# Optimization experiments

Hardware: AMD Instinct MI355X
Metric: run time of the kernel (lower is better)

## Reference

```python
import jax, jax.numpy as jnp
import numpy as np

N, T, F, D, E = 50000, 16, 128, 128, 1_600_000


def setup_inputs() -> dict:
    key = jax.random.key(0)
    k0, k1, k2, k3 = jax.random.split(key, 4)
    x = jax.random.normal(k0, (N, T, F), dtype=jnp.float32)
    edge_index = jax.random.randint(k1, (2, E), 0, N, dtype=jnp.int64)
    W_conv = jax.random.normal(k2, (F, D), dtype=jnp.float32) * 0.05
    b_conv = jnp.zeros((D,), dtype=jnp.float32)
    W_lin = jax.random.normal(k3, (D, D), dtype=jnp.float32) * 0.05
    b_lin = jnp.zeros((D,), dtype=jnp.float32)
    return {"x": x, "edge_index": edge_index, "W_conv": W_conv,
            "b_conv": b_conv, "W_lin": W_lin, "b_lin": b_lin}


def reference(x, edge_index, W_conv, b_conv, W_lin, b_lin):
    n = x.shape[0]
    loop = jnp.arange(n, dtype=edge_index.dtype)
    # GCNConv with add_self_loops=True (PyG semantics)
    src = jnp.concatenate([edge_index[0], loop])  # [E+N]
    dst = jnp.concatenate([edge_index[1], loop])  # [E+N]
    deg = jax.ops.segment_sum(jnp.ones_like(src, dtype=x.dtype), dst,
                              num_segments=n)
    dinv = jnp.where(deg > 0, jax.lax.rsqrt(deg), 0.0)
    norm = (dinv[src] * dinv[dst])[:, None]  # symmetric normalization

    def step(h_prev, xt):
        xw = xt @ W_conv                        # [N, D]
        agg = jax.ops.segment_sum(xw[src] * norm, dst, num_segments=n)
        h = jnp.tanh(agg + b_conv + h_prev @ W_lin + b_lin)
        return h, h

    h0 = jnp.zeros((n, W_conv.shape[1]), dtype=x.dtype)
    _, hs = jax.lax.scan(step, h0, jnp.swapaxes(x, 0, 1))  # hs: [T, N, D]
    return jnp.swapaxes(hs, 0, 1)  # [N, T, D]
```

## Files before the change

kernel.cpp:

```cpp
#include <hip/hip_runtime.h>
#include <math.h>

#define NN 50000
#define TT 16
#define DD 128
#define MT (NN * TT)
#define SCAN_B 1024
#define SCAN_NB ((NN + SCAN_B - 1) / SCAN_B)

typedef __attribute__((ext_vector_type(8))) short short8;
typedef __attribute__((ext_vector_type(4))) float f32x4;

static __device__ __forceinline__ unsigned short f2bf(float f) {
  unsigned u = __float_as_uint(f);
  u += 0x7FFFu + ((u >> 16) & 1u);
  return (unsigned short)(u >> 16);
}
static __device__ __forceinline__ float bf_lo(unsigned v) {
  return __uint_as_float(v << 16);
}
static __device__ __forceinline__ float bf_hi(unsigned v) {
  return __uint_as_float(v & 0xffff0000u);
}


__global__ void k_init(int* __restrict__ deg, int* __restrict__ cur) {
  int i = blockIdx.x * blockDim.x + threadIdx.x;
  if (i < NN) { deg[i] = 1; cur[i] = 0; }
}

__global__ void k_deg_count(const int* __restrict__ dst, int* __restrict__ deg, int e) {
  int i = blockIdx.x * blockDim.x + threadIdx.x;
  if (i < e) atomicAdd(&deg[dst[i]], 1);
}

__global__ __launch_bounds__(SCAN_B) void k_scan1(const int* __restrict__ deg,
                                                  int* __restrict__ rowptr,
                                                  int* __restrict__ bsums,
                                                  float* __restrict__ dinv) {
  __shared__ int sm[SCAN_B];
  int tid = threadIdx.x;
  int i = blockIdx.x * SCAN_B + tid;
  int d = (i < NN) ? deg[i] : 1;
  if (i < NN) dinv[i] = rsqrtf((float)d);
  int v = d - 1;
  sm[tid] = v;
  __syncthreads();
  for (int off = 1; off < SCAN_B; off <<= 1) {
    int t = (tid >= off) ? sm[tid - off] : 0;
    __syncthreads();
    sm[tid] += t;
    __syncthreads();
  }
  if (i < NN) rowptr[i] = sm[tid] - v;
  if (tid == SCAN_B - 1) bsums[blockIdx.x] = sm[tid];
}

__global__ void k_scan2(int* __restrict__ bsums) {
  __shared__ int sm[64];
  int tid = threadIdx.x;
  int v = (tid < SCAN_NB) ? bsums[tid] : 0;
  sm[tid] = v;
  __syncthreads();
  for (int off = 1; off < 64; off <<= 1) {
    int t = (tid >= off) ? sm[tid - off] : 0;
    __syncthreads();
    sm[tid] += t;
    __syncthreads();
  }
  if (tid < SCAN_NB) bsums[tid] = sm[tid] - v;
  if (tid == 63) bsums[SCAN_NB] = sm[63];
}

__global__ __launch_bounds__(SCAN_B) void k_scan3(int* __restrict__ rowptr,
                                                  const int* __restrict__ bsums) {
  int i = blockIdx.x * SCAN_B + threadIdx.x;
  if (i < NN) rowptr[i] += bsums[blockIdx.x];
  if (i == 0) rowptr[NN] = bsums[SCAN_NB];
}

__global__ void k_fill(const int* __restrict__ src, const int* __restrict__ dst,
                       const int* __restrict__ rowptr, int* __restrict__ cur,
                       int* __restrict__ col, int e) {
  int i = blockIdx.x * blockDim.x + threadIdx.x;
  if (i < e) {
    int d = dst[i];
    int slot = atomicAdd(&cur[d], 1);
    col[rowptr[d] + slot] = src[i];
  }
}

__global__ void k_wprep(const float* __restrict__ Wc, const float* __restrict__ Wl,
                        const float* __restrict__ bc, const float* __restrict__ bl,
                        unsigned short* __restrict__ Wct, unsigned short* __restrict__ Wlt,
                        float* __restrict__ bsum) {
  int n = blockIdx.x, k = threadIdx.x;
  Wct[n * 128 + k] = f2bf(Wc[k * 128 + n]);
  Wlt[n * 128 + k] = f2bf(Wl[k * 128 + n]);
  if (n == 0) bsum[k] = bc[k] + bl[k];
}

__global__ __launch_bounds__(256) void k_gemmx(
    const float* __restrict__ X, const unsigned short* __restrict__ Wct,
    const float* __restrict__ dinv, char* __restrict__ Yq, float* __restrict__ scaleN)
{
  __shared__ unsigned short sA[128 * 136];
  const int tid = threadIdx.x;
  const long row0 = (long)blockIdx.x * 128;

  {
    const float4* xp = (const float4*)(X + row0 * 128);
    #pragma unroll
    for (int it = 0; it < 16; ++it) {
      float4 v = xp[it * 256 + tid];
      int q = it * 256 + tid;
      int r = q >> 5;
      int k = (q & 31) * 4;
      unsigned u0 = (unsigned)f2bf(v.x) | ((unsigned)f2bf(v.y) << 16);
      unsigned u1 = (unsigned)f2bf(v.z) | ((unsigned)f2bf(v.w) << 16);
      *(uint2*)&sA[r * 136 + k] = make_uint2(u0, u1);
    }
  }
  __syncthreads();

  const int w = tid >> 6, l = tid & 63;
  const int lr = l & 15;
  const int lk = (l >> 4) << 3;
  f32x4 acc[2][8];
  #pragma unroll
  for (int i = 0; i < 2; ++i)
    #pragma unroll
    for (int n = 0; n < 8; ++n) acc[i][n] = (f32x4){0.f, 0.f, 0.f, 0.f};

  #pragma unroll
  for (int kg = 0; kg < 4; ++kg) {
    int kb = kg * 32 + lk;
    short8 a0 = *(const short8*)&sA[(w * 32 + lr) * 136 + kb];
    short8 a1 = *(const short8*)&sA[(w * 32 + 16 + lr) * 136 + kb];
    #pragma unroll
    for (int n = 0; n < 8; ++n) {
      short8 b = *(const short8*)&Wct[(n * 16 + lr) * 128 + kb];
      acc[0][n] = __builtin_amdgcn_mfma_f32_16x16x32_bf16(b, a0, acc[0][n], 0, 0, 0);
      acc[1][n] = __builtin_amdgcn_mfma_f32_16x16x32_bf16(b, a1, acc[1][n], 0, 0, 0);
    }
  }

  const int wb = (l >> 4) * 4;
  #pragma unroll
  for (int i = 0; i < 2; ++i) {
    const long rbase = row0 + w * 32 + i * 16;
    const int node = (int)(rbase >> 4);
    const long row = rbase + lr;
    float m = 0.f;
    #pragma unroll
    for (int n = 0; n < 8; ++n)
      #pragma unroll
      for (int r = 0; r < 4; ++r) m = fmaxf(m, fabsf(acc[i][n][r]));
    #pragma unroll
    for (int mask = 1; mask < 64; mask <<= 1)
      m = fmaxf(m, __shfl_xor(m, mask, 64));
    const float f = (m > 0.f) ? 127.f / m : 0.f;
    if (l == 0) scaleN[node] = m * dinv[node] * (1.f / 127.f);
    #pragma unroll
    for (int n = 0; n < 8; ++n) {
      int q0 = (int)__builtin_rintf(acc[i][n][0] * f);
      int q1 = (int)__builtin_rintf(acc[i][n][1] * f);
      int q2 = (int)__builtin_rintf(acc[i][n][2] * f);
      int q3 = (int)__builtin_rintf(acc[i][n][3] * f);
      unsigned u = (unsigned)(q0 & 255) | ((unsigned)(q1 & 255) << 8) |
                   ((unsigned)(q2 & 255) << 16) | ((unsigned)(q3 & 255) << 24);
      *(unsigned*)(Yq + row * 128 + n * 16 + wb) = u;
    }
  }
}

__global__ __launch_bounds__(256) void k_gatherN(
    const uint2* __restrict__ Yq,
    const float* __restrict__ scaleN,
    const int* __restrict__ col, const int* __restrict__ rowptr,
    const float* __restrict__ dinv, const float* __restrict__ bsum,
    unsigned* __restrict__ aggT)
{
  const int n = blockIdx.x;
  const int tid = threadIdx.x;
  float a0 = 0, a1 = 0, a2 = 0, a3 = 0, a4 = 0, a5 = 0, a6 = 0, a7 = 0;
  {
    uint2 v = Yq[(long)n * 256 + tid];
    float ss = scaleN[n];
    a0 = fmaf((float)(signed char)(v.x),       ss, a0);
    a1 = fmaf((float)(signed char)(v.x >> 8),  ss, a1);
    a2 = fmaf((float)(signed char)(v.x >> 16), ss, a2);
    a3 = fmaf((float)(signed char)(v.x >> 24), ss, a3);
    a4 = fmaf((float)(signed char)(v.y),       ss, a4);
    a5 = fmaf((float)(signed char)(v.y >> 8),  ss, a5);
    a6 = fmaf((float)(signed char)(v.y >> 16), ss, a6);
    a7 = fmaf((float)(signed char)(v.y >> 24), ss, a7);
  }
  int j = rowptr[n];
  const int end = rowptr[n + 1];
  for (; j + 4 <= end; j += 4) {
    int s0 = col[j], s1 = col[j + 1], s2 = col[j + 2], s3 = col[j + 3];
    float c0 = scaleN[s0], c1 = scaleN[s1], c2 = scaleN[s2], c3 = scaleN[s3];
    uint2 v0 = Yq[(long)s0 * 256 + tid];
    uint2 v1 = Yq[(long)s1 * 256 + tid];
    uint2 v2 = Yq[(long)s2 * 256 + tid];
    uint2 v3 = Yq[(long)s3 * 256 + tid];
    a0 = fmaf((float)(signed char)(v0.x),       c0, a0);
    a1 = fmaf((float)(signed char)(v0.x >> 8),  c0, a1);
    a2 = fmaf((float)(signed char)(v0.x >> 16), c0, a2);
    a3 = fmaf((float)(signed char)(v0.x >> 24), c0, a3);
    a4 = fmaf((float)(signed char)(v0.y),       c0, a4);
    a5 = fmaf((float)(signed char)(v0.y >> 8),  c0, a5);
    a6 = fmaf((float)(signed char)(v0.y >> 16), c0, a6);
    a7 = fmaf((float)(signed char)(v0.y >> 24), c0, a7);
    a0 = fmaf((float)(signed char)(v1.x),       c1, a0);
    a1 = fmaf((float)(signed char)(v1.x >> 8),  c1, a1);
    a2 = fmaf((float)(signed char)(v1.x >> 16), c1, a2);
    a3 = fmaf((float)(signed char)(v1.x >> 24), c1, a3);
    a4 = fmaf((float)(signed char)(v1.y),       c1, a4);
    a5 = fmaf((float)(signed char)(v1.y >> 8),  c1, a5);
    a6 = fmaf((float)(signed char)(v1.y >> 16), c1, a6);
    a7 = fmaf((float)(signed char)(v1.y >> 24), c1, a7);
    a0 = fmaf((float)(signed char)(v2.x),       c2, a0);
    a1 = fmaf((float)(signed char)(v2.x >> 8),  c2, a1);
    a2 = fmaf((float)(signed char)(v2.x >> 16), c2, a2);
    a3 = fmaf((float)(signed char)(v2.x >> 24), c2, a3);
    a4 = fmaf((float)(signed char)(v2.y),       c2, a4);
    a5 = fmaf((float)(signed char)(v2.y >> 8),  c2, a5);
    a6 = fmaf((float)(signed char)(v2.y >> 16), c2, a6);
    a7 = fmaf((float)(signed char)(v2.y >> 24), c2, a7);
    a0 = fmaf((float)(signed char)(v3.x),       c3, a0);
    a1 = fmaf((float)(signed char)(v3.x >> 8),  c3, a1);
    a2 = fmaf((float)(signed char)(v3.x >> 16), c3, a2);
    a3 = fmaf((float)(signed char)(v3.x >> 24), c3, a3);
    a4 = fmaf((float)(signed char)(v3.y),       c3, a4);
    a5 = fmaf((float)(signed char)(v3.y >> 8),  c3, a5);
    a6 = fmaf((float)(signed char)(v3.y >> 16), c3, a6);
    a7 = fmaf((float)(signed char)(v3.y >> 24), c3, a7);
  }
  for (; j < end; ++j) {
    int s = col[j];
    float cs = scaleN[s];
    uint2 v = Yq[(long)s * 256 + tid];
    a0 = fmaf((float)(signed char)(v.x),       cs, a0);
    a1 = fmaf((float)(signed char)(v.x >> 8),  cs, a1);
    a2 = fmaf((float)(signed char)(v.x >> 16), cs, a2);
    a3 = fmaf((float)(signed char)(v.x >> 24), cs, a3);
    a4 = fmaf((float)(signed char)(v.y),       cs, a4);
    a5 = fmaf((float)(signed char)(v.y >> 8),  cs, a5);
    a6 = fmaf((float)(signed char)(v.y >> 16), cs, a6);
    a7 = fmaf((float)(signed char)(v.y >> 24), cs, a7);
  }
  const int t = tid >> 4, dq = tid & 15;
  const float di = dinv[n];
  const float4 b0 = *(const float4*)&bsum[dq * 8];
  const float4 b1 = *(const float4*)&bsum[dq * 8 + 4];
  a0 = fmaf(a0, di, b0.x); a1 = fmaf(a1, di, b0.y);
  a2 = fmaf(a2, di, b0.z); a3 = fmaf(a3, di, b0.w);
  a4 = fmaf(a4, di, b1.x); a5 = fmaf(a5, di, b1.y);
  a6 = fmaf(a6, di, b1.z); a7 = fmaf(a7, di, b1.w);
  unsigned u0 = (unsigned)f2bf(a0) | ((unsigned)f2bf(a1) << 16);
  unsigned u1 = (unsigned)f2bf(a2) | ((unsigned)f2bf(a3) << 16);
  unsigned u2 = (unsigned)f2bf(a4) | ((unsigned)f2bf(a5) << 16);
  unsigned u3 = (unsigned)f2bf(a6) | ((unsigned)f2bf(a7) << 16);
  unsigned* ap = aggT + ((long)t * NN + n) * 64 + dq * 4;
  __builtin_nontemporal_store(u0, ap);
  __builtin_nontemporal_store(u1, ap + 1);
  __builtin_nontemporal_store(u2, ap + 2);
  __builtin_nontemporal_store(u3, ap + 3);
}

__global__ __launch_bounds__(64) void k_rnn(
    const unsigned* __restrict__ aggT,
    const unsigned short* __restrict__ Wlt,
    float* __restrict__ out)
{
  __shared__ unsigned sag[16 * 72];
  __shared__ unsigned short hl[16 * 144];
  __shared__ float ob[16 * 132];
  const int l = threadIdx.x;
  const int lr = l & 15, lg = l >> 4;
  const long nbase = (long)blockIdx.x * 16;

  short8 wf[4][8];
  #pragma unroll
  for (int kg = 0; kg < 4; ++kg)
    #pragma unroll
    for (int n = 0; n < 8; ++n)
      wf[kg][n] = *(const short8*)&Wlt[(n * 16 + lr) * 128 + kg * 32 + lg * 8];

  uint4 g[4];
  {
    const uint4* src = (const uint4*)(aggT + nbase * 64);
    #pragma unroll
    for (int i = 0; i < 4; ++i) g[i] = src[i * 64 + l];
    #pragma unroll
    for (int i = 0; i < 4; ++i) {
      int gi = (i * 64 + l) * 4;
      *(uint4*)&sag[(gi >> 6) * 72 + (gi & 63)] = g[i];
    }
  }
  {
    const uint4* src = (const uint4*)(aggT + ((long)NN + nbase) * 64);
    #pragma unroll
    for (int i = 0; i < 4; ++i) g[i] = src[i * 64 + l];
  }
  __syncthreads();
  #pragma unroll
  for (int n = 0; n < 8; ++n) {
    uint2 ag = *(const uint2*)&sag[lr * 72 + n * 8 + lg * 2];
    float o0 = tanhf(bf_lo(ag.x));
    float o1 = tanhf(bf_hi(ag.x));
    float o2 = tanhf(bf_lo(ag.y));
    float o3 = tanhf(bf_hi(ag.y));
    *(float4*)&ob[lr * 132 + n * 16 + lg * 4] = make_float4(o0, o1, o2, o3);
    unsigned u0 = (unsigned)f2bf(o0) | ((unsigned)f2bf(o1) << 16);
    unsigned u1 = (unsigned)f2bf(o2) | ((unsigned)f2bf(o3) << 16);
    *(uint2*)&hl[lr * 144 + n * 16 + lg * 4] = make_uint2(u0, u1);
  }
  __syncthreads();
  #pragma unroll
  for (int i = 0; i < 8; ++i) {
    int r2 = i * 2 + (l >> 5);
    int c = (l & 31) * 4;
    float4 v = *(const float4*)&ob[r2 * 132 + c];
    *(float4*)(out + ((nbase + r2) * TT) * 128 + c) = v;
  }

  for (int t = 1; t < TT; ++t) {
    #pragma unroll
    for (int i = 0; i < 4; ++i) {
      int gi = (i * 64 + l) * 4;
      *(uint4*)&sag[(gi >> 6) * 72 + (gi & 63)] = g[i];
    }
    if (t + 1 < TT) {
      const uint4* src = (const uint4*)(aggT + ((long)(t + 1) * NN + nbase) * 64);
      #pragma unroll
      for (int i = 0; i < 4; ++i) g[i] = src[i * 64 + l];
    }
    short8 bfr[4];
    #pragma unroll
    for (int kg = 0; kg < 4; ++kg)
      bfr[kg] = *(const short8*)&hl[lr * 144 + kg * 32 + lg * 8];
    __syncthreads();

    f32x4 acc[8];
    #pragma unroll
    for (int n = 0; n < 8; ++n) acc[n] = (f32x4){0.f, 0.f, 0.f, 0.f};
    #pragma unroll
    for (int kg = 0; kg < 4; ++kg) {
      #pragma unroll
      for (int n = 0; n < 8; ++n)
        acc[n] = __builtin_amdgcn_mfma_f32_16x16x32_bf16(wf[kg][n], bfr[kg], acc[n], 0, 0, 0);
    }
    #pragma unroll
    for (int n = 0; n < 8; ++n) {
      uint2 ag = *(const uint2*)&sag[lr * 72 + n * 8 + lg * 2];
      float o0 = tanhf(acc[n][0] + bf_lo(ag.x));
      float o1 = tanhf(acc[n][1] + bf_hi(ag.x));
      float o2 = tanhf(acc[n][2] + bf_lo(ag.y));
      float o3 = tanhf(acc[n][3] + bf_hi(ag.y));
      *(float4*)&ob[lr * 132 + n * 16 + lg * 4] = make_float4(o0, o1, o2, o3);
      unsigned u0 = (unsigned)f2bf(o0) | ((unsigned)f2bf(o1) << 16);
      unsigned u1 = (unsigned)f2bf(o2) | ((unsigned)f2bf(o3) << 16);
      *(uint2*)&hl[lr * 144 + n * 16 + lg * 4] = make_uint2(u0, u1);
    }
    __syncthreads();
    #pragma unroll
    for (int i = 0; i < 8; ++i) {
      int r2 = i * 2 + (l >> 5);
      int c = (l & 31) * 4;
      float4 v = *(const float4*)&ob[r2 * 132 + c];
      *(float4*)(out + ((nbase + r2) * TT + t) * 128 + c) = v;
    }
  }
}

extern "C" void kernel_launch(void* const* d_in, const int* in_sizes, int n_in,
                              void* d_out, int out_size, void* d_ws, size_t ws_size,
                              hipStream_t stream) {
  const float* x  = (const float*)d_in[0];
  const int*   ei = (const int*)d_in[1];
  const float* Wc = (const float*)d_in[2];
  const float* bc = (const float*)d_in[3];
  const float* Wl = (const float*)d_in[4];
  const float* bl = (const float*)d_in[5];
  float* out = (float*)d_out;
  const int E = in_sizes[1] / 2;
  const int* srcp = ei;
  const int* dstp = ei + E;

  char* w = (char*)d_ws;
  auto alloc = [&](size_t bytes) {
    char* p = w;
    w += (bytes + 255) & ~(size_t)255;
    return p;
  };
  int*            deg    = (int*)alloc(sizeof(int) * NN);
  float*          dinv   = (float*)alloc(sizeof(float) * NN);
  int*            rowptr = (int*)alloc(sizeof(int) * (NN + 1));
  int*            cur    = (int*)alloc(sizeof(int) * NN);
  int*            bsums  = (int*)alloc(sizeof(int) * (SCAN_NB + 1));
  int*            col    = (int*)alloc(sizeof(int) * (size_t)E);
  char*           Yq     = (char*)alloc((size_t)MT * DD);
  float*          scaleN = (float*)alloc(sizeof(float) * NN);
  unsigned*       aggT   = (unsigned*)alloc(sizeof(unsigned) * (size_t)MT * 64);
  float*          bsum   = (float*)alloc(sizeof(float) * DD);
  unsigned short* Wct    = (unsigned short*)alloc(sizeof(unsigned short) * 128 * 128);
  unsigned short* Wlt    = (unsigned short*)alloc(sizeof(unsigned short) * 128 * 128);

  k_init<<<(NN + 255) / 256, 256, 0, stream>>>(deg, cur);
  k_deg_count<<<(E + 255) / 256, 256, 0, stream>>>(dstp, deg, E);
  k_scan1<<<SCAN_NB, SCAN_B, 0, stream>>>(deg, rowptr, bsums, dinv);
  k_scan2<<<1, 64, 0, stream>>>(bsums);
  k_scan3<<<SCAN_NB, SCAN_B, 0, stream>>>(rowptr, bsums);
  k_fill<<<(E + 255) / 256, 256, 0, stream>>>(srcp, dstp, rowptr, cur, col, E);
  k_wprep<<<128, 128, 0, stream>>>(Wc, Wl, bc, bl, Wct, Wlt, bsum);

  k_gemmx<<<MT / 128, 256, 0, stream>>>(x, Wct, dinv, Yq, scaleN);
  k_gatherN<<<NN, 256, 0, stream>>>((const uint2*)Yq, scaleN, col, rowptr, dinv, bsum, aggT);
  k_rnn<<<NN / 16, 64, 0, stream>>>(aggT, Wlt, out);
}
```

Measured before the change: 1.034 ms.

## Fuse degree counting into GEMM grid and merge init with weight prep

Init and weight-transpose prep now run as one launch, split across block ranges. The edge degree-count atomics are appended as extra blocks to the input GEMM grid, so they run alongside the MFMA work. Because degrees are no longer known when the GEMM runs, the per-node dinv scaling of the quantization scale moves into the scan3 kernel. This cuts two launches and overlaps the atomic pass with compute, at the cost of an extra read-modify-write of scaleN.

```diff
diff --git a/kernel.cpp b/kernel.cpp
--- a/kernel.cpp
+++ b/kernel.cpp
@@ -23,15 +23,102 @@
   return __uint_as_float(v & 0xffff0000u);
 }
 
-
-__global__ void k_init(int* __restrict__ deg, int* __restrict__ cur) {
-  int i = blockIdx.x * blockDim.x + threadIdx.x;
-  if (i < NN) { deg[i] = 1; cur[i] = 0; }
-}
-
-__global__ void k_deg_count(const int* __restrict__ dst, int* __restrict__ deg, int e) {
-  int i = blockIdx.x * blockDim.x + threadIdx.x;
-  if (i < e) atomicAdd(&deg[dst[i]], 1);
+__global__ void k_init_prep(int* __restrict__ deg, int* __restrict__ cur,
+                            const float* __restrict__ Wc, const float* __restrict__ Wl,
+                            const float* __restrict__ bc, const float* __restrict__ bl,
+                            unsigned short* __restrict__ Wct, unsigned short* __restrict__ Wlt,
+                            float* __restrict__ bsum) {
+  const int b = blockIdx.x;
+  if (b < 196) {
+    int i = b * 256 + threadIdx.x;
+    if (i < NN) { deg[i] = 1; cur[i] = 0; }
+  } else {
+    int n = (b - 196) * 2 + (threadIdx.x >> 7);
+    int k = threadIdx.x & 127;
+    Wct[n * 128 + k] = f2bf(Wc[k * 128 + n]);
+    Wlt[n * 128 + k] = f2bf(Wl[k * 128 + n]);
+    if (n == 0) bsum[k] = bc[k] + bl[k];
+  }
+}
+
+__global__ __launch_bounds__(256) void k_gemmx_deg(
+    const float* __restrict__ X, const unsigned short* __restrict__ Wct,
+    char* __restrict__ Yq, float* __restrict__ scaleN,
+    const int* __restrict__ dst, int* __restrict__ deg, int E, int gx)
+{
+  __shared__ unsigned short sA[128 * 136];
+  const int tid = threadIdx.x;
+  if ((int)blockIdx.x >= gx) {
+    int i = ((int)blockIdx.x - gx) * 256 + tid;
+    if (i < E) atomicAdd(&deg[dst[i]], 1);
+    return;
+  }
+  const long row0 = (long)blockIdx.x * 128;
+
+  {
+    const float4* xp = (const float4*)(X + row0 * 128);
+    #pragma unroll
+    for (int it = 0; it < 16; ++it) {
+      float4 v = xp[it * 256 + tid];
+      int q = it * 256 + tid;
+      int r = q >> 5;
+      int k = (q & 31) * 4;
+      unsigned u0 = (unsigned)f2bf(v.x) | ((unsigned)f2bf(v.y) << 16);
+      unsigned u1 = (unsigned)f2bf(v.z) | ((unsigned)f2bf(v.w) << 16);
+      *(uint2*)&sA[r * 136 + k] = make_uint2(u0, u1);
+    }
+  }
+  __syncthreads();
+
+  const int w = tid >> 6, l = tid & 63;
+  const int lr = l & 15;
+  const int lk = (l >> 4) << 3;
+  f32x4 acc[2][8];
+  #pragma unroll
+  for (int i = 0; i < 2; ++i)
+    #pragma unroll
+    for (int n = 0; n < 8; ++n) acc[i][n] = (f32x4){0.f, 0.f, 0.f, 0.f};
+
+  #pragma unroll
+  for (int kg = 0; kg < 4; ++kg) {
+    int kb = kg * 32 + lk;
+    short8 a0 = *(const short8*)&sA[(w * 32 + lr) * 136 + kb];
+    short8 a1 = *(const short8*)&sA[(w * 32 + 16 + lr) * 136 + kb];
+    #pragma unroll
+    for (int n = 0; n < 8; ++n) {
+      short8 b = *(const short8*)&Wct[(n * 16 + lr) * 128 + kb];
+      acc[0][n] = __builtin_amdgcn_mfma_f32_16x16x32_bf16(b, a0, acc[0][n], 0, 0, 0);
+      acc[1][n] = __builtin_amdgcn_mfma_f32_16x16x32_bf16(b, a1, acc[1][n], 0, 0, 0);
+    }
+  }
+
+  const int wb = (l >> 4) * 4;
+  #pragma unroll
+  for (int i = 0; i < 2; ++i) {
+    const long rbase = row0 + w * 32 + i * 16;
+    const int node = (int)(rbase >> 4);
+    const long row = rbase + lr;
+    float m = 0.f;
+    #pragma unroll
+    for (int n = 0; n < 8; ++n)
+      #pragma unroll
+      for (int r = 0; r < 4; ++r) m = fmaxf(m, fabsf(acc[i][n][r]));
+    #pragma unroll
+    for (int mask = 1; mask < 64; mask <<= 1)
+      m = fmaxf(m, __shfl_xor(m, mask, 64));
+    const float f = (m > 0.f) ? 127.f / m : 0.f;
+    if (l == 0) scaleN[node] = m * (1.f / 127.f);
+    #pragma unroll
+    for (int n = 0; n < 8; ++n) {
+      int q0 = (int)__builtin_rintf(acc[i][n][0] * f);
+      int q1 = (int)__builtin_rintf(acc[i][n][1] * f);
+      int q2 = (int)__builtin_rintf(acc[i][n][2] * f);
+      int q3 = (int)__builtin_rintf(acc[i][n][3] * f);
+      unsigned u = (unsigned)(q0 & 255) | ((unsigned)(q1 & 255) << 8) |
+                   ((unsigned)(q2 & 255) << 16) | ((unsigned)(q3 & 255) << 24);
+      *(unsigned*)(Yq + row * 128 + n * 16 + wb) = u;
+    }
+  }
 }
 
 __global__ __launch_bounds__(SCAN_B) void k_scan1(const int* __restrict__ deg,
@@ -73,9 +160,14 @@
 }
 
 __global__ __launch_bounds__(SCAN_B) void k_scan3(int* __restrict__ rowptr,
-                                                  const int* __restrict__ bsums) {
+                                                  const int* __restrict__ bsums,
+                                                  float* __restrict__ scaleN,
+                                                  const float* __restrict__ dinv) {
   int i = blockIdx.x * SCAN_B + threadIdx.x;
-  if (i < NN) rowptr[i] += bsums[blockIdx.x];
+  if (i < NN) {
+    rowptr[i] += bsums[blockIdx.x];
+    scaleN[i] *= dinv[i];
+  }
   if (i == 0) rowptr[NN] = bsums[SCAN_NB];
 }
 
@@ -87,90 +179,6 @@
     int d = dst[i];
     int slot = atomicAdd(&cur[d], 1);
     col[rowptr[d] + slot] = src[i];
-  }
-}
-
-__global__ void k_wprep(const float* __restrict__ Wc, const float* __restrict__ Wl,
-                        const float* __restrict__ bc, const float* __restrict__ bl,
-                        unsigned short* __restrict__ Wct, unsigned short* __restrict__ Wlt,
-                        float* __restrict__ bsum) {
-  int n = blockIdx.x, k = threadIdx.x;
-  Wct[n * 128 + k] = f2bf(Wc[k * 128 + n]);
-  Wlt[n * 128 + k] = f2bf(Wl[k * 128 + n]);
-  if (n == 0) bsum[k] = bc[k] + bl[k];
-}
-
-__global__ __launch_bounds__(256) void k_gemmx(
-    const float* __restrict__ X, const unsigned short* __restrict__ Wct,
-    const float* __restrict__ dinv, char* __restrict__ Yq, float* __restrict__ scaleN)
-{
-  __shared__ unsigned short sA[128 * 136];
-  const int tid = threadIdx.x;
-  const long row0 = (long)blockIdx.x * 128;
-
-  {
-    const float4* xp = (const float4*)(X + row0 * 128);
-    #pragma unroll
-    for (int it = 0; it < 16; ++it) {
-      float4 v = xp[it * 256 + tid];
-      int q = it * 256 + tid;
-      int r = q >> 5;
-      int k = (q & 31) * 4;
-      unsigned u0 = (unsigned)f2bf(v.x) | ((unsigned)f2bf(v.y) << 16);
-      unsigned u1 = (unsigned)f2bf(v.z) | ((unsigned)f2bf(v.w) << 16);
-      *(uint2*)&sA[r * 136 + k] = make_uint2(u0, u1);
-    }
-  }
-  __syncthreads();
-
-  const int w = tid >> 6, l = tid & 63;
-  const int lr = l & 15;
-  const int lk = (l >> 4) << 3;
-  f32x4 acc[2][8];
-  #pragma unroll
-  for (int i = 0; i < 2; ++i)
-    #pragma unroll
-    for (int n = 0; n < 8; ++n) acc[i][n] = (f32x4){0.f, 0.f, 0.f, 0.f};
-
-  #pragma unroll
-  for (int kg = 0; kg < 4; ++kg) {
-    int kb = kg * 32 + lk;
-    short8 a0 = *(const short8*)&sA[(w * 32 + lr) * 136 + kb];
-    short8 a1 = *(const short8*)&sA[(w * 32 + 16 + lr) * 136 + kb];
-    #pragma unroll
-    for (int n = 0; n < 8; ++n) {
-      short8 b = *(const short8*)&Wct[(n * 16 + lr) * 128 + kb];
-      acc[0][n] = __builtin_amdgcn_mfma_f32_16x16x32_bf16(b, a0, acc[0][n], 0, 0, 0);
-      acc[1][n] = __builtin_amdgcn_mfma_f32_16x16x32_bf16(b, a1, acc[1][n], 0, 0, 0);
-    }
-  }
-
-  const int wb = (l >> 4) * 4;
-  #pragma unroll
-  for (int i = 0; i < 2; ++i) {
-    const long rbase = row0 + w * 32 + i * 16;
-    const int node = (int)(rbase >> 4);
-    const long row = rbase + lr;
-    float m = 0.f;
-    #pragma unroll
-    for (int n = 0; n < 8; ++n)
-      #pragma unroll
-      for (int r = 0; r < 4; ++r) m = fmaxf(m, fabsf(acc[i][n][r]));
-    #pragma unroll
-    for (int mask = 1; mask < 64; mask <<= 1)
-      m = fmaxf(m, __shfl_xor(m, mask, 64));
-    const float f = (m > 0.f) ? 127.f / m : 0.f;
-    if (l == 0) scaleN[node] = m * dinv[node] * (1.f / 127.f);
-    #pragma unroll
-    for (int n = 0; n < 8; ++n) {
-      int q0 = (int)__builtin_rintf(acc[i][n][0] * f);
-      int q1 = (int)__builtin_rintf(acc[i][n][1] * f);
-      int q2 = (int)__builtin_rintf(acc[i][n][2] * f);
-      int q3 = (int)__builtin_rintf(acc[i][n][3] * f);
-      unsigned u = (unsigned)(q0 & 255) | ((unsigned)(q1 & 255) << 8) |
-                   ((unsigned)(q2 & 255) << 16) | ((unsigned)(q3 & 255) << 24);
-      *(unsigned*)(Yq + row * 128 + n * 16 + wb) = u;
-    }
   }
 }
 
@@ -409,15 +417,15 @@
   unsigned short* Wct    = (unsigned short*)alloc(sizeof(unsigned short) * 128 * 128);
   unsigned short* Wlt    = (unsigned short*)alloc(sizeof(unsigned short) * 128 * 128);
 
-  k_init<<<(NN + 255) / 256, 256, 0, stream>>>(deg, cur);
-  k_deg_count<<<(E + 255) / 256, 256, 0, stream>>>(dstp, deg, E);
+  const int degB = (E + 255) / 256;
+  const int gx = MT / 128;
+
+  k_init_prep<<<260, 256, 0, stream>>>(deg, cur, Wc, Wl, bc, bl, Wct, Wlt, bsum);
+  k_gemmx_deg<<<gx + degB, 256, 0, stream>>>(x, Wct, Yq, scaleN, dstp, deg, E, gx);
   k_scan1<<<SCAN_NB, SCAN_B, 0, stream>>>(deg, rowptr, bsums, dinv);
   k_scan2<<<1, 64, 0, stream>>>(bsums);
-  k_scan3<<<SCAN_NB, SCAN_B, 0, stream>>>(rowptr, bsums);
-  k_fill<<<(E + 255) / 256, 256, 0, stream>>>(srcp, dstp, rowptr, cur, col, E);
-  k_wprep<<<128, 128, 0, stream>>>(Wc, Wl, bc, bl, Wct, Wlt, bsum);
-
-  k_gemmx<<<MT / 128, 256, 0, stream>>>(x, Wct, dinv, Yq, scaleN);
+  k_scan3<<<SCAN_NB, SCAN_B, 0, stream>>>(rowptr, bsums, scaleN, dinv);
+  k_fill<<<degB, 256, 0, stream>>>(srcp, dstp, rowptr, cur, col, E);
   k_gatherN<<<NN, 256, 0, stream>>>((const uint2*)Yq, scaleN, col, rowptr, dinv, bsum, aggT);
   k_rnn<<<NN / 16, 64, 0, stream>>>(aggT, Wlt, out);
 }
```

Result: faster. 1.005 ms (-2.8%).
